# Optimization experiments

Measured on AMD Instinct MI355X. Metric: run time of the kernel, lower is better.

## Reference

```python
import jax, jax.numpy as jnp
import numpy as np

B, C, H, W = 16, 256, 56, 56
NH = 8           # num_heads
BS = 8           # block_size
HALO = 3         # halo_size
WIN = BS + 2 * HALO   # 14
MLP = 4


def setup_inputs() -> dict:
    key = jax.random.key(0)
    ks = jax.random.split(key, 8)
    f = lambda k, shape, s: jax.random.normal(k, shape, jnp.float32) * s
    return dict(
        x=jax.random.normal(ks[0], (B, C, H, W), jnp.float32),
        ln1_g=jnp.ones((C,), jnp.float32), ln1_b=jnp.zeros((C,), jnp.float32),
        wq=f(ks[1], (C, C), C ** -0.5), bq=jnp.zeros((C,), jnp.float32),
        wkv=f(ks[2], (2 * C, C), C ** -0.5), bkv=jnp.zeros((2 * C,), jnp.float32),
        bias=f(ks[3], (1, NH, 1, BS * BS, WIN * WIN), 0.02),
        gamma1=jnp.full((1, C, 1, 1), 1e-6, jnp.float32),
        ln2_g=jnp.ones((C,), jnp.float32), ln2_b=jnp.zeros((C,), jnp.float32),
        w1=f(ks[4], (MLP * C, C), 0.02), b1=jnp.zeros((MLP * C,), jnp.float32),
        w2=f(ks[5], (C, MLP * C), 0.02), b2=jnp.zeros((C,), jnp.float32),
        gamma2=jnp.full((1, 1, 1, C), 1e-6, jnp.float32),
    )


def _ln2d(x, g, b, eps=1e-5):
    # LayerNorm over channel dim of NCHW
    mu = jnp.mean(x, axis=1, keepdims=True)
    var = jnp.mean((x - mu) ** 2, axis=1, keepdims=True)
    return (x - mu) * jax.lax.rsqrt(var + eps) * g[None, :, None, None] + b[None, :, None, None]


def _halo_attn(x, wq, bq, wkv, bkv, bias):
    Bn, Cc, Hh, Ww = x.shape
    dh = Cc // NH
    scale = dh ** -0.5
    nHb, nWb = Hh // BS, Ww // BS
    xh = jnp.transpose(x, (0, 2, 3, 1))            # B,H,W,C
    q = xh @ wq.T + bq                             # 1x1 conv
    kv = xh @ wkv.T + bkv                          # B,H,W,2C
    # q blocks: B,nh,nblocks,bs^2,dh
    q = q.reshape(Bn, nHb, BS, nWb, BS, NH, dh).transpose(0, 5, 1, 3, 2, 4, 6)
    q = q.reshape(Bn, NH, nHb * nWb, BS * BS, dh)
    # kv halo windows
    kvp = jnp.pad(kv, ((0, 0), (HALO, HALO), (HALO, HALO), (0, 0)))
    ih = (jnp.arange(nHb) * BS)[:, None] + jnp.arange(WIN)[None, :]
    iw = (jnp.arange(nWb) * BS)[:, None] + jnp.arange(WIN)[None, :]
    kvw = kvp[:, ih[:, None, :, None], iw[None, :, None, :], :]
    kvw = kvw.reshape(Bn, nHb * nWb, WIN * WIN, NH, 2 * dh).transpose(0, 3, 1, 2, 4)
    k, v = kvw[..., :dh], kvw[..., dh:]
    attn = jnp.einsum('bhnqd,bhnkd->bhnqk', q, k) * scale + bias
    attn = jax.nn.softmax(attn, axis=-1)
    out = jnp.einsum('bhnqk,bhnkd->bhnqd', attn, v)                   # B,nh,nb,bs^2,dh
    out = out.reshape(Bn, NH, nHb, nWb, BS, BS, dh).transpose(0, 1, 6, 2, 4, 3, 5)
    return out.reshape(Bn, Cc, Hh, Ww)


def _forward(x, ln1_g, ln1_b, wq, bq, wkv, bkv, bias, gamma1,
             ln2_g, ln2_b, w1, b1, w2, b2, gamma2):
    shortcut = x
    a = _halo_attn(_ln2d(x, ln1_g, ln1_b), wq, bq, wkv, bkv, bias)
    x = shortcut + gamma1 * a
    shortcut = x
    y = jnp.transpose(_ln2d(x, ln2_g, ln2_b), (0, 2, 3, 1))           # NHWC
    y = jax.nn.gelu(y @ w1.T + b1, approximate=False) @ w2.T + b2
    y = gamma2 * y
    return shortcut + jnp.transpose(y, (0, 3, 1, 2))


def reference(x, ln1_g, ln1_b, wq, bq, wkv, bkv, bias, gamma1,
              ln2_g, ln2_b, w1, b1, w2, b2, gamma2):
    return _forward(x, ln1_g, ln1_b, wq, bq, wkv, bkv, bias, gamma1,
                    ln2_g, ln2_b, w1, b1, w2, b2, gamma2)
```

## Files before the change

kernel.cpp:

```cpp
#include <hip/hip_runtime.h>
#include <hip/hip_bf16.h>
#include <math.h>

typedef unsigned short u16;
typedef float f32x4 __attribute__((ext_vector_type(4)));
typedef __bf16 bf16x8 __attribute__((ext_vector_type(8)));

__device__ __forceinline__ float bf2f(u16 u) {
    union { float f; unsigned int i; } v; v.i = ((unsigned int)u) << 16; return v.f;
}
__device__ __forceinline__ u16 f2bf(float f) {
    union { float f; unsigned int i; } v; v.f = f;
    unsigned int x = v.i;
    return (u16)((x + 0x7FFFu + ((x >> 16) & 1u)) >> 16);
}
__device__ __forceinline__ unsigned int cvt_pk_bf16(float lo, float hi) {
    unsigned int r;
    asm("v_cvt_pk_bf16_f32 %0, %1, %2" : "=v"(r) : "v"(lo), "v"(hi));
    return r;
}

__global__ __launch_bounds__(256) void k_prep(const float* __restrict__ wq, const float* __restrict__ wkv,
                                              const float* __restrict__ w1, const float* __restrict__ w2,
                                              u16* __restrict__ wqkvb, u16* __restrict__ w1p, u16* __restrict__ w2p) {
    const int bid = blockIdx.x, t = threadIdx.x;
    if (bid < 192) {
        int e = (bid * 256 + t) * 4;
        const float* src = (e < 65536) ? (wq + e) : (wkv + (e - 65536));
        float sc = (e < 65536) ? 0.17677669529663687f : 1.f;
        float4 v = *(const float4*)src;
        ushort4 o;
        o.x = f2bf(v.x * sc); o.y = f2bf(v.y * sc); o.z = f2bf(v.z * sc); o.w = f2bf(v.w * sc);
        *(ushort4*)(wqkvb + e) = o;
    } else if (bid < 320) {
        int tid = (bid - 192) * 256 + t;
        int kc = tid >> 11, rem = tid & 2047;
        int wave = rem >> 9, rem2 = rem & 511;
        int ks = rem2 >> 6, lane = rem2 & 63;
        int ln = lane & 15, quad = lane >> 4;
        const float* src = w1 + (size_t)(kc * 64 + wave * 16 + ln) * 256 + ks * 32 + quad * 8;
        float4 v0 = *(const float4*)src;
        float4 v1 = *(const float4*)(src + 4);
        alignas(16) u16 tmp[8];
        tmp[0] = f2bf(v0.x); tmp[1] = f2bf(v0.y); tmp[2] = f2bf(v0.z); tmp[3] = f2bf(v0.w);
        tmp[4] = f2bf(v1.x); tmp[5] = f2bf(v1.y); tmp[6] = f2bf(v1.z); tmp[7] = f2bf(v1.w);
        *(int4*)(w1p + (size_t)tid * 8) = *(int4*)tmp;
    } else {
        int tid = (bid - 320) * 256 + t;
        int kc = tid >> 11, rem = tid & 2047;
        int wave = rem >> 9, rem2 = rem & 511;
        int ks2 = rem2 >> 8, rem3 = rem2 & 255;
        int nt = rem3 >> 6, lane = rem3 & 63;
        int ln = lane & 15, quad = lane >> 4;
        const float* src = w2 + (size_t)(wave * 64 + nt * 16 + ln) * 1024 + kc * 64 + ks2 * 32 + quad * 8;
        float4 v0 = *(const float4*)src;
        float4 v1 = *(const float4*)(src + 4);
        alignas(16) u16 tmp[8];
        tmp[0] = f2bf(v0.x); tmp[1] = f2bf(v0.y); tmp[2] = f2bf(v0.z); tmp[3] = f2bf(v0.w);
        tmp[4] = f2bf(v1.x); tmp[5] = f2bf(v1.y); tmp[6] = f2bf(v1.z); tmp[7] = f2bf(v1.w);
        *(int4*)(w2p + (size_t)tid * 8) = *(int4*)tmp;
    }
}

__global__ __launch_bounds__(256) void k_transpose(const float* __restrict__ x, u16* __restrict__ xh) {
    __shared__ __align__(16) u16 tile[64][72];
    const int t = threadIdx.x;
    const int hw0 = blockIdx.x * 64;
    const int c0  = blockIdx.y * 64;
    const int b   = blockIdx.z;
    const int cl = t >> 2, wl = (t & 3) * 16;
    {
        int c = c0 + cl;
        const float* src = x + (size_t)(b * 256 + c) * 3136 + hw0 + wl;
        for (int q = 0; q < 4; q++) {
            float4 v = *(const float4*)(src + q * 4);
            u16* dst = &tile[cl][wl + q * 4];
            dst[0] = f2bf(v.x); dst[1] = f2bf(v.y); dst[2] = f2bf(v.z); dst[3] = f2bf(v.w);
        }
    }
    __syncthreads();
    const int hl = t >> 3, cl2 = (t & 7) * 8;
    for (int i = 0; i < 2; i++) {
        int hw = hl + i * 32;
        alignas(16) u16 tmp[8];
        for (int j = 0; j < 8; j++) tmp[j] = tile[cl2 + j][hw];
        u16* dst = xh + (size_t)(b * 3136 + hw0 + hw) * 256 + c0 + cl2;
        *(int4*)dst = *(int4*)tmp;
    }
}

__global__ __launch_bounds__(256) void k_ln(const u16* __restrict__ in, u16* __restrict__ out,
                                            const float* __restrict__ g, const float* __restrict__ bta) {
    const int wave = threadIdx.x >> 6, lane = threadIdx.x & 63;
    const int p = blockIdx.x * 4 + wave;
    ushort4 v = *(const ushort4*)(in + (size_t)p * 256 + lane * 4);
    float f0 = bf2f(v.x), f1 = bf2f(v.y), f2 = bf2f(v.z), f3 = bf2f(v.w);
    float s = f0 + f1 + f2 + f3;
    float sq = f0 * f0 + f1 * f1 + f2 * f2 + f3 * f3;
    for (int o = 32; o >= 1; o >>= 1) { s += __shfl_xor(s, o, 64); sq += __shfl_xor(sq, o, 64); }
    float m = s * (1.f / 256.f);
    float var = sq * (1.f / 256.f) - m * m;
    float inv = rsqrtf(var + 1e-5f);
    float4 gv = *(const float4*)(g + lane * 4);
    float4 bv = *(const float4*)(bta + lane * 4);
    ushort4 o4;
    o4.x = f2bf((f0 - m) * inv * gv.x + bv.x);
    o4.y = f2bf((f1 - m) * inv * gv.y + bv.y);
    o4.z = f2bf((f2 - m) * inv * gv.z + bv.z);
    o4.w = f2bf((f3 - m) * inv * gv.w + bv.w);
    *(ushort4*)(out + (size_t)p * 256 + lane * 4) = o4;
}

__global__ __launch_bounds__(256) void k_qkv(
    const u16* __restrict__ xn, const u16* __restrict__ Bw,
    const float* __restrict__ bq, const float* __restrict__ bkv,
    u16* __restrict__ out) {
    __shared__ __align__(16) u16 smem[17408];
    u16* As = smem;
    u16* Bs = smem + 4096;

    const int g = blockIdx.x;
    const int xcd = g & 7, idx = g >> 3;
    const int bm = xcd * 49 + idx / 6, bn = idx % 6;

    const int t = threadIdx.x;
    const int wave = t >> 6, lane = t & 63;
    const int wm = (wave >> 1) * 64, wn = (wave & 1) * 64;
    const int ln = lane & 15, quad = lane >> 4;

    f32x4 vzero = {0.f, 0.f, 0.f, 0.f};
    f32x4 acc[4][4];
    for (int i = 0; i < 4; i++) for (int j = 0; j < 4; j++) acc[i][j] = vzero;

    const int srow = t >> 2;
    const int scol = (t & 3) * 8;

    for (int k0 = 0; k0 < 256; k0 += 32) {
        for (int i = 0; i < 2; i++) {
            int r = srow + i * 64;
            *(int4*)&As[r * 32 + scol] = *(const int4*)(xn + (size_t)(bm * 128 + r) * 256 + k0 + scol);
            *(int4*)&Bs[r * 32 + scol] = *(const int4*)(Bw + (size_t)(bn * 128 + r) * 256 + k0 + scol);
        }
        __syncthreads();
        bf16x8 af[4], bfr[4];
        for (int mt = 0; mt < 4; mt++) af[mt] = *(const bf16x8*)&As[(wm + mt * 16 + ln) * 32 + quad * 8];
        for (int nt = 0; nt < 4; nt++) bfr[nt] = *(const bf16x8*)&Bs[(wn + nt * 16 + ln) * 32 + quad * 8];
        for (int mt = 0; mt < 4; mt++)
            for (int nt = 0; nt < 4; nt++)
                acc[mt][nt] = __builtin_amdgcn_mfma_f32_16x16x32_bf16(bfr[nt], af[mt], acc[mt][nt], 0, 0, 0);
        __syncthreads();
    }

    u16* Cs = smem;
    for (int nt = 0; nt < 4; nt++) {
        int gn0 = bn * 128 + wn + nt * 16 + quad * 4;
        f32x4 bv;
        if (gn0 < 256) {
            f32x4 tq = *(const f32x4*)(bq + gn0);
            bv = tq * 0.17677669529663687f;
        } else {
            bv = *(const f32x4*)(bkv + gn0 - 256);
        }
        for (int mt = 0; mt < 4; mt++) {
            ushort4 pk;
            pk.x = f2bf(acc[mt][nt][0] + bv[0]);
            pk.y = f2bf(acc[mt][nt][1] + bv[1]);
            pk.z = f2bf(acc[mt][nt][2] + bv[2]);
            pk.w = f2bf(acc[mt][nt][3] + bv[3]);
            *(ushort4*)&Cs[(wm + mt * 16 + ln) * 136 + wn + nt * 16 + quad * 4] = pk;
        }
    }
    __syncthreads();
    const int row = t >> 4, col = (t & 15) * 8;
    for (int pass = 0; pass < 8; pass++) {
        int rr = pass * 16 + row;
        int4 v = *(int4*)&Cs[rr * 136 + col];
        *(int4*)(out + (size_t)(bm * 128 + rr) * 768 + bn * 128 + col) = v;
    }
}

__global__ __launch_bounds__(256, 3) void k_mlp(
    const u16* __restrict__ xn, const u16* __restrict__ x2,
    const u16* __restrict__ w1p, const float* __restrict__ b1,
    const u16* __restrict__ w2p, const float* __restrict__ b2,
    const float* __restrict__ g2v, float* __restrict__ outT) {
    __shared__ __align__(16) u16 smem[16896 + 8704];
    u16* As = smem;
    u16* Hs = smem + 16896;

    const int g = blockIdx.x;
    const int bm = (g & 7) * 98 + (g >> 3);

    const int t = threadIdx.x;
    const int wave = t >> 6, lane = t & 63;
    const int ln = lane & 15, quad = lane >> 4;
    const int wn64 = wave * 64;
    const int wq4 = wave * 2;

    f32x4 vzero = {0.f, 0.f, 0.f, 0.f};
    f32x4 acc[4][4];
    for (int i = 0; i < 4; i++) for (int j = 0; j < 4; j++) acc[i][j] = vzero;

    {
        const int srow = t >> 2, scb = (t & 3) * 8;
        for (int c = 0; c < 8; c++) {
            int col = scb + c * 32;
            *(int4*)&As[srow * 264 + col] = *(const int4*)(xn + (size_t)(bm * 64 + srow) * 256 + col);
        }
    }
    __syncthreads();

    for (int kc = 0; kc < 8; kc++) {
        bf16x8 w1f[2][8];
        {
            const u16* w1b = w1p + (size_t)(kc * 8 + wq4) * 4096 + lane * 8;
            #pragma unroll
            for (int nt = 0; nt < 2; nt++)
                #pragma unroll
                for (int ks = 0; ks < 8; ks++)
                    w1f[nt][ks] = *(const bf16x8*)(w1b + nt * 4096 + ks * 512);
        }
        f32x4 up[4][2];
        #pragma unroll
        for (int i = 0; i < 4; i++) { up[i][0] = vzero; up[i][1] = vzero; }
        #pragma unroll
        for (int ks = 0; ks < 8; ks++) {
            #pragma unroll
            for (int mt = 0; mt < 4; mt++) {
                bf16x8 af = *(const bf16x8*)&As[(mt * 16 + ln) * 264 + ks * 32 + quad * 8];
                up[mt][0] = __builtin_amdgcn_mfma_f32_16x16x32_bf16(w1f[0][ks], af, up[mt][0], 0, 0, 0);
                up[mt][1] = __builtin_amdgcn_mfma_f32_16x16x32_bf16(w1f[1][ks], af, up[mt][1], 0, 0, 0);
            }
        }
        bf16x8 w2f[4][4];
        #pragma unroll
        for (int ks2 = 0; ks2 < 4; ks2++) {
            const u16* w2b = w2p + (size_t)((((kc * 2 + (ks2 >> 1)) * 4 + wave) * 2 + (ks2 & 1)) * 4) * 512 + lane * 8;
            #pragma unroll
            for (int nt = 0; nt < 4; nt++)
                w2f[ks2][nt] = *(const bf16x8*)(w2b + nt * 512);
        }
        __syncthreads();
        #pragma unroll
        for (int nt = 0; nt < 2; nt++) {
            float4 bv = *(const float4*)(b1 + kc * 128 + wave * 32 + nt * 16 + quad * 4);
            #pragma unroll
            for (int mt = 0; mt < 4; mt++) {
                float v0 = up[mt][nt][0] + bv.x;
                float v1 = up[mt][nt][1] + bv.y;
                float v2 = up[mt][nt][2] + bv.z;
                float v3 = up[mt][nt][3] + bv.w;
                uint2 pk;
                pk.x = cvt_pk_bf16(v0 * (1.f / (1.f + __expf(-1.702f * v0))),
                                   v1 * (1.f / (1.f + __expf(-1.702f * v1))));
                pk.y = cvt_pk_bf16(v2 * (1.f / (1.f + __expf(-1.702f * v2))),
                                   v3 * (1.f / (1.f + __expf(-1.702f * v3))));
                *(uint2*)&Hs[(mt * 16 + ln) * 136 + wave * 32 + nt * 16 + quad * 4] = pk;
            }
        }
        __syncthreads();
        #pragma unroll
        for (int ks2 = 0; ks2 < 4; ks2++) {
            bf16x8 hf[4];
            #pragma unroll
            for (int mt = 0; mt < 4; mt++)
                hf[mt] = *(const bf16x8*)&Hs[(mt * 16 + ln) * 136 + ks2 * 32 + quad * 8];
            #pragma unroll
            for (int nt = 0; nt < 4; nt++) {
                #pragma unroll
                for (int mt = 0; mt < 4; mt++)
                    acc[mt][nt] = __builtin_amdgcn_mfma_f32_16x16x32_bf16(hf[mt], w2f[ks2][nt], acc[mt][nt], 0, 0, 0);
            }
        }
    }

    const int b = bm / 49;
    for (int nt = 0; nt < 4; nt++) {
        int gn = wn64 + nt * 16 + ln;
        float bs = b2[gn], g2 = g2v[gn];
        for (int mt = 0; mt < 4; mt++) {
            int gm0 = bm * 64 + mt * 16 + quad * 4;
            int hw0 = gm0 - b * 3136;
            f32x4 res;
            for (int r = 0; r < 4; r++)
                res[r] = bf2f(x2[(size_t)(gm0 + r) * 256 + gn]) + g2 * (acc[mt][nt][r] + bs);
            *(f32x4*)(outT + (size_t)(b * 256 + gn) * 3136 + hw0) = res;
        }
    }
}

__global__ __launch_bounds__(256, 4) void k_attn(
    const u16* __restrict__ qkv, const float* __restrict__ bias,
    const u16* __restrict__ xh, const float* __restrict__ gamma1,
    u16* __restrict__ x2) {
    __shared__ __align__(16) u16 Kl[208 * 40];
    __shared__ __align__(16) u16 Vt[32 * 236];

    const int t = threadIdx.x;
    const int blk = blockIdx.x, head = blockIdx.y, b = blockIdx.z;
    const int bh = blk / 7, bw = blk - bh * 7;
    const int wave = t >> 6, lane = t & 63;
    const int ln = lane & 15, quad = lane >> 4;

    for (int cid = t; cid < 208 * 8; cid += 256) {
        int pos = cid >> 3, part = cid & 7;
        int i = pos / 14, j = pos - i * 14;
        int gh = bh * 8 - 3 + i, gw = bw * 8 - 3 + j;
        bool valid = (pos < 196) && ((unsigned)gh < 56u) && ((unsigned)gw < 56u);
        int d0 = (part & 3) * 8;
        int4 v = {0, 0, 0, 0};
        if (valid) {
            size_t p = (size_t)(b * 56 + gh) * 56 + gw;
            v = *(const int4*)(qkv + p * 768 + 256 + head * 64 + ((part & 4) ? 32 : 0) + d0);
        }
        if (!(part & 4)) {
            *(int4*)&Kl[pos * 40 + d0] = v;
        } else {
            alignas(16) u16 tmp[8];
            *(int4*)tmp = v;
            for (int jj = 0; jj < 8; jj++) Vt[(d0 + jj) * 236 + pos] = tmp[jj];
        }
    }
    __syncthreads();

    const int qrow = wave * 16 + ln;
    const int qh = bh * 8 + (qrow >> 3), qw = bw * 8 + (qrow & 7);
    const size_t qp = (size_t)(b * 56 + qh) * 56 + qw;
    bf16x8 qf = *(const bf16x8*)(qkv + qp * 768 + head * 32 + quad * 8);

    f32x4 s[13];
    const float* bp = bias + (size_t)(head * 64 + qrow) * 196 + quad * 4;
    #pragma unroll
    for (int nt = 0; nt < 13; nt++) {
        bf16x8 kf = *(const bf16x8*)&Kl[(nt * 16 + ln) * 40 + quad * 8];
        f32x4 c;
        if (nt < 12 || quad == 0) {
            c = *(const f32x4*)(bp + nt * 16);
        } else {
            c = (f32x4){-1e30f, -1e30f, -1e30f, -1e30f};
        }
        s[nt] = __builtin_amdgcn_mfma_f32_16x16x32_bf16(kf, qf, c, 0, 0, 0);
    }

    float mx = -1e30f;
    #pragma unroll
    for (int nt = 0; nt < 13; nt++)
        #pragma unroll
        for (int r = 0; r < 4; r++) mx = fmaxf(mx, s[nt][r]);
    mx = fmaxf(mx, __shfl_xor(mx, 16, 64));
    mx = fmaxf(mx, __shfl_xor(mx, 32, 64));
    float sum = 0.f;
    #pragma unroll
    for (int nt = 0; nt < 13; nt++)
        #pragma unroll
        for (int r = 0; r < 4; r++) {
            float e = __expf(s[nt][r] - mx);
            s[nt][r] = e;
            sum += e;
        }
    sum += __shfl_xor(sum, 16, 64);
    sum += __shfl_xor(sum, 32, 64);
    float rinv = 1.f / sum;

    unsigned int pk[13][2];
    #pragma unroll
    for (int nt = 0; nt < 13; nt++) {
        pk[nt][0] = cvt_pk_bf16(s[nt][0], s[nt][1]);
        pk[nt][1] = cvt_pk_bf16(s[nt][2], s[nt][3]);
    }

    f32x4 vzero = {0.f, 0.f, 0.f, 0.f};
    f32x4 o_acc[2];
    o_acc[0] = vzero; o_acc[1] = vzero;
    #pragma unroll
    for (int kc = 0; kc < 7; kc++) {
        union { int4 i4; bf16x8 v; } pu;
        pu.i4.x = pk[2 * kc][0];
        pu.i4.y = pk[2 * kc][1];
        pu.i4.z = (kc < 6) ? pk[2 * kc + 1][0] : 0;
        pu.i4.w = (kc < 6) ? pk[2 * kc + 1][1] : 0;
        #pragma unroll
        for (int n2 = 0; n2 < 2; n2++) {
            union { int4 i4; bf16x8 v; } vu;
            const u16* vb = &Vt[(n2 * 16 + ln) * 236 + kc * 32 + quad * 4];
            *(int2*)&vu.i4.x = *(const int2*)vb;
            if (kc < 6) {
                *(int2*)&vu.i4.z = *(const int2*)(vb + 16);
            } else {
                vu.i4.z = 0; vu.i4.w = 0;
            }
            o_acc[n2] = __builtin_amdgcn_mfma_f32_16x16x32_bf16(pu.v, vu.v, o_acc[n2], 0, 0, 0);
        }
    }

    float rr4[4];
    #pragma unroll
    for (int r = 0; r < 4; r++) rr4[r] = __shfl(rinv, quad * 4 + r, 16);

    #pragma unroll
    for (int n2 = 0; n2 < 2; n2++) {
        int c = head * 32 + n2 * 16 + ln;
        float g1 = gamma1[c];
        #pragma unroll
        for (int r = 0; r < 4; r++) {
            int q = wave * 16 + quad * 4 + r;
            int hh = bh * 8 + (q >> 3), ww = bw * 8 + (q & 7);
            size_t p = (size_t)(b * 56 + hh) * 56 + ww;
            float a = o_acc[n2][r] * rr4[r];
            x2[p * 256 + c] = f2bf(bf2f(xh[p * 256 + c]) + g1 * a);
        }
    }
}

extern "C" void kernel_launch(void* const* d_in, const int* in_sizes, int n_in,
                              void* d_out, int out_size, void* d_ws, size_t ws_size,
                              hipStream_t stream) {
    const float* x      = (const float*)d_in[0];
    const float* ln1_g  = (const float*)d_in[1];
    const float* ln1_b  = (const float*)d_in[2];
    const float* wq     = (const float*)d_in[3];
    const float* bq     = (const float*)d_in[4];
    const float* wkv    = (const float*)d_in[5];
    const float* bkv    = (const float*)d_in[6];
    const float* bias   = (const float*)d_in[7];
    const float* gamma1 = (const float*)d_in[8];
    const float* ln2_g  = (const float*)d_in[9];
    const float* ln2_b  = (const float*)d_in[10];
    const float* w1     = (const float*)d_in[11];
    const float* b1     = (const float*)d_in[12];
    const float* w2     = (const float*)d_in[13];
    const float* b2     = (const float*)d_in[14];
    const float* gamma2 = (const float*)d_in[15];

    char* ws = (char*)d_ws;
    u16* qkv   = (u16*)ws;
    u16* xh    = (u16*)(ws + 77070336);
    u16* x2    = (u16*)(ws + 102760448);
    u16* wqkvb = (u16*)(ws + 128450560);
    u16* w1p   = (u16*)(ws + 128843776);
    u16* w2p   = (u16*)(ws + 129368064);
    u16* xn1   = x2;
    u16* xn2   = xh;

    k_prep<<<dim3(448), 256, 0, stream>>>(wq, wkv, w1, w2, wqkvb, w1p, w2p);
    k_transpose<<<dim3(49, 4, 16), 256, 0, stream>>>(x, xh);
    k_ln<<<dim3(12544), 256, 0, stream>>>(xh, xn1, ln1_g, ln1_b);
    k_qkv<<<dim3(2352), 256, 0, stream>>>(xn1, wqkvb, bq, bkv, qkv);
    k_attn<<<dim3(49, 8, 16), 256, 0, stream>>>(qkv, bias, xh, gamma1, x2);
    k_ln<<<dim3(12544), 256, 0, stream>>>(x2, xn2, ln2_g, ln2_b);
    k_mlp<<<dim3(784), 256, 0, stream>>>(xn2, x2, w1p, b1, w2p, b2, gamma2, (float*)d_out);
}
```

Baseline: 357.6 us.

## Fuse second LayerNorm into MLP kernel and double-buffer hidden tile

Removes the separate LN2 kernel launch by computing the per-row mean and variance inside k_mlp's A-tile load, reading x2 directly and writing normalized bf16 into shared memory. The hidden-activation buffer Hs becomes double-buffered across kc iterations, so one __syncthreads per iteration can be dropped. Scalar bf16 rounding is also replaced with the packed v_cvt_pk_bf16 instruction in the transpose, LN and QKV epilogues. The larger shared allocation and the removal of the occupancy hint of 3 in launch_bounds may lower occupancy of the MLP kernel.

```diff
diff --git a/kernel.cpp b/kernel.cpp
--- a/kernel.cpp
+++ b/kernel.cpp
@@ -74,8 +74,10 @@
         const float* src = x + (size_t)(b * 256 + c) * 3136 + hw0 + wl;
         for (int q = 0; q < 4; q++) {
             float4 v = *(const float4*)(src + q * 4);
-            u16* dst = &tile[cl][wl + q * 4];
-            dst[0] = f2bf(v.x); dst[1] = f2bf(v.y); dst[2] = f2bf(v.z); dst[3] = f2bf(v.w);
+            uint2 pr;
+            pr.x = cvt_pk_bf16(v.x, v.y);
+            pr.y = cvt_pk_bf16(v.z, v.w);
+            *(uint2*)&tile[cl][wl + q * 4] = pr;
         }
     }
     __syncthreads();
@@ -103,12 +105,10 @@
     float inv = rsqrtf(var + 1e-5f);
     float4 gv = *(const float4*)(g + lane * 4);
     float4 bv = *(const float4*)(bta + lane * 4);
-    ushort4 o4;
-    o4.x = f2bf((f0 - m) * inv * gv.x + bv.x);
-    o4.y = f2bf((f1 - m) * inv * gv.y + bv.y);
-    o4.z = f2bf((f2 - m) * inv * gv.z + bv.z);
-    o4.w = f2bf((f3 - m) * inv * gv.w + bv.w);
-    *(ushort4*)(out + (size_t)p * 256 + lane * 4) = o4;
+    uint2 o2;
+    o2.x = cvt_pk_bf16((f0 - m) * inv * gv.x + bv.x, (f1 - m) * inv * gv.y + bv.y);
+    o2.y = cvt_pk_bf16((f2 - m) * inv * gv.z + bv.z, (f3 - m) * inv * gv.w + bv.w);
+    *(uint2*)(out + (size_t)p * 256 + lane * 4) = o2;
 }
 
 __global__ __launch_bounds__(256) void k_qkv(
@@ -162,12 +162,10 @@
             bv = *(const f32x4*)(bkv + gn0 - 256);
         }
         for (int mt = 0; mt < 4; mt++) {
-            ushort4 pk;
-            pk.x = f2bf(acc[mt][nt][0] + bv[0]);
-            pk.y = f2bf(acc[mt][nt][1] + bv[1]);
-            pk.z = f2bf(acc[mt][nt][2] + bv[2]);
-            pk.w = f2bf(acc[mt][nt][3] + bv[3]);
-            *(ushort4*)&Cs[(wm + mt * 16 + ln) * 136 + wn + nt * 16 + quad * 4] = pk;
+            uint2 pk2;
+            pk2.x = cvt_pk_bf16(acc[mt][nt][0] + bv[0], acc[mt][nt][1] + bv[1]);
+            pk2.y = cvt_pk_bf16(acc[mt][nt][2] + bv[2], acc[mt][nt][3] + bv[3]);
+            *(uint2*)&Cs[(wm + mt * 16 + ln) * 136 + wn + nt * 16 + quad * 4] = pk2;
         }
     }
     __syncthreads();
@@ -179,14 +177,15 @@
     }
 }
 
-__global__ __launch_bounds__(256, 3) void k_mlp(
-    const u16* __restrict__ xn, const u16* __restrict__ x2,
+__global__ __launch_bounds__(256) void k_mlp(
+    const u16* __restrict__ x2,
     const u16* __restrict__ w1p, const float* __restrict__ b1,
     const u16* __restrict__ w2p, const float* __restrict__ b2,
-    const float* __restrict__ g2v, float* __restrict__ outT) {
-    __shared__ __align__(16) u16 smem[16896 + 8704];
+    const float* __restrict__ g2v,
+    const float* __restrict__ ln2g, const float* __restrict__ ln2b,
+    float* __restrict__ outT) {
+    __shared__ __align__(16) u16 smem[16896 + 2 * 8704];
     u16* As = smem;
-    u16* Hs = smem + 16896;
 
     const int g = blockIdx.x;
     const int bm = (g & 7) * 98 + (g >> 3);
@@ -203,14 +202,54 @@
 
     {
         const int srow = t >> 2, scb = (t & 3) * 8;
+        const u16* src = x2 + (size_t)(bm * 64 + srow) * 256;
+        int4 raw[8];
+        #pragma unroll
+        for (int c = 0; c < 8; c++) raw[c] = *(const int4*)(src + scb + c * 32);
+        float s = 0.f, sq = 0.f;
+        #pragma unroll
+        for (int c = 0; c < 8; c++) {
+            const unsigned int* u = (const unsigned int*)&raw[c];
+            #pragma unroll
+            for (int k = 0; k < 4; k++) {
+                union { unsigned int i; float f; } lo, hi;
+                lo.i = u[k] << 16; hi.i = u[k] & 0xFFFF0000u;
+                s += lo.f + hi.f;
+                sq += lo.f * lo.f + hi.f * hi.f;
+            }
+        }
+        s  += __shfl_xor(s, 1, 64);  s  += __shfl_xor(s, 2, 64);
+        sq += __shfl_xor(sq, 1, 64); sq += __shfl_xor(sq, 2, 64);
+        float m = s * (1.f / 256.f);
+        float var = sq * (1.f / 256.f) - m * m;
+        float inv = rsqrtf(var + 1e-5f);
+        #pragma unroll
         for (int c = 0; c < 8; c++) {
             int col = scb + c * 32;
-            *(int4*)&As[srow * 264 + col] = *(const int4*)(xn + (size_t)(bm * 64 + srow) * 256 + col);
+            float4 gv0 = *(const float4*)(ln2g + col);
+            float4 gv1 = *(const float4*)(ln2g + col + 4);
+            float4 bv0 = *(const float4*)(ln2b + col);
+            float4 bv1 = *(const float4*)(ln2b + col + 4);
+            const unsigned int* u = (const unsigned int*)&raw[c];
+            float f[8];
+            #pragma unroll
+            for (int k = 0; k < 4; k++) {
+                union { unsigned int i; float f; } lo, hi;
+                lo.i = u[k] << 16; hi.i = u[k] & 0xFFFF0000u;
+                f[2 * k] = lo.f; f[2 * k + 1] = hi.f;
+            }
+            uint4 o;
+            o.x = cvt_pk_bf16((f[0] - m) * inv * gv0.x + bv0.x, (f[1] - m) * inv * gv0.y + bv0.y);
+            o.y = cvt_pk_bf16((f[2] - m) * inv * gv0.z + bv0.z, (f[3] - m) * inv * gv0.w + bv0.w);
+            o.z = cvt_pk_bf16((f[4] - m) * inv * gv1.x + bv1.x, (f[5] - m) * inv * gv1.y + bv1.y);
+            o.w = cvt_pk_bf16((f[6] - m) * inv * gv1.z + bv1.z, (f[7] - m) * inv * gv1.w + bv1.w);
+            *(uint4*)&As[srow * 264 + col] = o;
         }
     }
     __syncthreads();
 
     for (int kc = 0; kc < 8; kc++) {
+        u16* Hs = smem + 16896 + (kc & 1) * 8704;
         bf16x8 w1f[2][8];
         {
             const u16* w1b = w1p + (size_t)(kc * 8 + wq4) * 4096 + lane * 8;
@@ -240,7 +279,6 @@
             for (int nt = 0; nt < 4; nt++)
                 w2f[ks2][nt] = *(const bf16x8*)(w2b + nt * 512);
         }
-        __syncthreads();
         #pragma unroll
         for (int nt = 0; nt < 2; nt++) {
             float4 bv = *(const float4*)(b1 + kc * 128 + wave * 32 + nt * 16 + quad * 4);
@@ -440,13 +478,11 @@
     u16* w1p   = (u16*)(ws + 128843776);
     u16* w2p   = (u16*)(ws + 129368064);
     u16* xn1   = x2;
-    u16* xn2   = xh;
 
     k_prep<<<dim3(448), 256, 0, stream>>>(wq, wkv, w1, w2, wqkvb, w1p, w2p);
     k_transpose<<<dim3(49, 4, 16), 256, 0, stream>>>(x, xh);
     k_ln<<<dim3(12544), 256, 0, stream>>>(xh, xn1, ln1_g, ln1_b);
     k_qkv<<<dim3(2352), 256, 0, stream>>>(xn1, wqkvb, bq, bkv, qkv);
     k_attn<<<dim3(49, 8, 16), 256, 0, stream>>>(qkv, bias, xh, gamma1, x2);
-    k_ln<<<dim3(12544), 256, 0, stream>>>(x2, xn2, ln2_g, ln2_b);
-    k_mlp<<<dim3(784), 256, 0, stream>>>(xn2, x2, w1p, b1, w2p, b2, gamma2, (float*)d_out);
-}
+    k_mlp<<<dim3(784), 256, 0, stream>>>(x2, w1p, b1, w2p, b2, gamma2, ln2_g, ln2_b, (float*)d_out);
+}
```

Result: slower. 383.5 us (+7.2%).
